# Performance work log

Measured on AMD Instinct MI355X. Metric: run time of the kernel, lower is better.

Reference implementation:

```python
import jax, jax.numpy as jnp
import numpy as np

B, S, D, H = 8, 1024, 1024, 16
HD = D // H  # 64


def setup_inputs() -> dict:
    key = jax.random.key(0)
    ks = jax.random.split(key, 10)
    s = 1.0 / np.sqrt(HD)
    x = jax.random.normal(ks[0], (B, S, D), dtype=jnp.float32)
    mask = jax.random.randint(ks[1], (B, S), 0, 2).astype(bool)  # True = padded
    # per-head q/k/v projections of SimpleAttention, stacked over heads
    Wq = jax.random.normal(ks[2], (H, HD, HD), dtype=jnp.float32) * s
    bq = jnp.zeros((H, HD), dtype=jnp.float32)
    Wk = jax.random.normal(ks[3], (H, HD, HD), dtype=jnp.float32) * s
    bk = jnp.zeros((H, HD), dtype=jnp.float32)
    Wv = jax.random.normal(ks[4], (H, HD, HD), dtype=jnp.float32) * s
    bv = jnp.zeros((H, HD), dtype=jnp.float32)
    # out_proj: Linear(dim, dim)
    Wo = jax.random.normal(ks[5], (D, D), dtype=jnp.float32) * (1.0 / np.sqrt(D))
    bo = jnp.zeros((D,), dtype=jnp.float32)
    return {"x": x, "mask": mask, "Wq": Wq, "bq": bq, "Wk": Wk, "bk": bk,
            "Wv": Wv, "bv": bv, "Wo": Wo, "bo": bo}


def reference(x, mask, Wq, bq, Wk, bk, Wv, bv, Wo, bo):
    b, s, d = x.shape
    xh = x.reshape(b, s, H, HD).transpose(0, 2, 1, 3)  # (b, h, s, hd)
    # per-head linear projections (batched over heads via einsum)
    q = jnp.einsum('bhsd,hde->bhse', xh, Wq) + bq[None, :, None, :]
    k = jnp.einsum('bhsd,hde->bhse', xh, Wk) + bk[None, :, None, :]
    v = jnp.einsum('bhsd,hde->bhse', xh, Wv) + bv[None, :, None, :]
    scale = 1.0 / jnp.sqrt(jnp.asarray(HD, dtype=x.dtype))
    scores = jnp.einsum('bhqd,bhkd->bhqk', q, k) * scale  # (b, h, s, s)
    # key-padding mask: True = padded -> -inf on key axis
    neg = jnp.asarray(jnp.finfo(x.dtype).min, dtype=x.dtype)
    scores = jnp.where(mask[:, None, None, :], neg, scores)
    attn = jax.nn.softmax(scores, axis=-1)
    out = jnp.einsum('bhqk,bhkd->bhqd', attn, v)  # (b, h, s, hd)
    concat = out.transpose(0, 2, 1, 3).reshape(b, s, d)
    # out_proj (dropout is identity in eval)
    return concat @ Wo.T + bo
```

## Files before the change

kernel.cpp:

```cpp
#include <hip/hip_runtime.h>
#include <float.h>

#define B_ 8
#define S_ 1024
#define D_ 1024
#define H_ 16
#define HD_ 64

typedef __attribute__((ext_vector_type(8))) _Float16 half8;
typedef __attribute__((ext_vector_type(4))) _Float16 half4;
typedef __attribute__((ext_vector_type(4))) float f32x4;

__device__ __forceinline__ void gld16(const void* g, void* l) {
  __builtin_amdgcn_global_load_lds(
      (const __attribute__((address_space(1))) void*)g,
      (__attribute__((address_space(3))) void*)l, 16, 0, 0);
}

__global__ __launch_bounds__(256) void prep_kernel(
    const float* __restrict__ Wq, const float* __restrict__ bq,
    const float* __restrict__ Wk, const float* __restrict__ bk,
    const float* __restrict__ Wv, const float* __restrict__ bv,
    const float* __restrict__ Wo, const void* __restrict__ mraw,
    _Float16* __restrict__ Wc, float* __restrict__ bs,
    _Float16* __restrict__ Wo16, float* __restrict__ maskadd) {
  const int bid = blockIdx.x;
  const int tid = threadIdx.x;
  if (bid < 768) {
    const int idx = bid * 256 + tid;
    const int d = idx & 63;
    const int e = (idx >> 6) & 63;
    const int t2 = idx >> 12;
    const int m = t2 % 3, h = t2 / 3;
    const int src = h * 4096 + d * 64 + e;
    float v = (m == 0) ? Wq[src] * 0.18033688f : (m == 1) ? Wk[src] : Wv[src];
    Wc[idx] = (_Float16)v;
    if (idx < 3072) {
      const int mm = idx >> 10, he = idx & 1023;
      float vv = (mm == 0) ? bq[he] * 0.18033688f : (mm == 1) ? bk[he] : bv[he];
      bs[idx] = vv;
    }
  } else if (bid < 800) {
    __shared__ int bad;
    if (tid == 0) bad = 0;
    __syncthreads();
    const unsigned int* mw = (const unsigned int*)mraw;
    int my = 0;
    for (int j = tid; j < 2048; j += 256) my |= (mw[j] & ~1u) ? 1 : 0;
    if (my) atomicOr(&bad, 1);
    __syncthreads();
    const int i = (bid - 768) * 256 + tid;
    const int f = bad;
    const int v = f ? (int)((const unsigned char*)mraw)[i] : ((const int*)mraw)[i];
    maskadd[i] = (v != 0) ? -FLT_MAX : 0.0f;
  } else {
    const int i = (bid - 800) * 256 + tid;
    Wo16[i] = (_Float16)Wo[i];
  }
}

__global__ __launch_bounds__(256) void qkv_kernel(
    const float* __restrict__ x, const _Float16* __restrict__ Wc,
    const float* __restrict__ bs,
    _Float16* __restrict__ q16, _Float16* __restrict__ k16, _Float16* __restrict__ vT16) {
  const int tile = blockIdx.x & 15;
  const int bh = blockIdx.x >> 4;
  const int b = bh >> 4, h = bh & 15;
  const int s0 = tile * 64;
  const int w = threadIdx.x >> 6, lane = threadIdx.x & 63;
  const int col = lane & 15, quad = lane >> 4;
  const int srow = s0 + w * 16 + col;

  const float* xr = x + ((size_t)(b * S_) + srow) * D_ + h * HD_;
  f32x4 x0a = *(const f32x4*)(xr + quad * 8);
  f32x4 x0b = *(const f32x4*)(xr + quad * 8 + 4);
  f32x4 x1a = *(const f32x4*)(xr + 32 + quad * 8);
  f32x4 x1b = *(const f32x4*)(xr + 32 + quad * 8 + 4);
  half8 Xf0, Xf1;
#pragma unroll
  for (int j = 0; j < 4; ++j) {
    Xf0[j] = (_Float16)x0a[j];
    Xf0[4 + j] = (_Float16)x0b[j];
    Xf1[j] = (_Float16)x1a[j];
    Xf1[4 + j] = (_Float16)x1b[j];
  }

  const _Float16* wbase = Wc + (size_t)h * 3 * 4096;
  const f32x4 z4 = {0.f, 0.f, 0.f, 0.f};
#pragma unroll
  for (int mm = 0; mm < 2; ++mm) {
    _Float16* outp = mm ? k16 : q16;
    const _Float16* wm = wbase + mm * 4096;
#pragma unroll
    for (int et = 0; et < 4; ++et) {
      const _Float16* wr = wm + (et * 16 + col) * 64;
      half8 W0 = *(const half8*)(wr + quad * 8);
      half8 W1 = *(const half8*)(wr + 32 + quad * 8);
      f32x4 c = __builtin_amdgcn_mfma_f32_16x16x32_f16(W0, Xf0, z4, 0, 0, 0);
      c = __builtin_amdgcn_mfma_f32_16x16x32_f16(W1, Xf1, c, 0, 0, 0);
      f32x4 bb = *(const f32x4*)(bs + mm * 1024 + h * 64 + et * 16 + quad * 4);
      half4 o;
#pragma unroll
      for (int r = 0; r < 4; ++r) o[r] = (_Float16)(c[r] + bb[r]);
      *(half4*)(outp + ((size_t)bh * S_ + srow) * HD_ + et * 16 + quad * 4) = o;
    }
  }
  {
    const _Float16* wm = wbase + 2 * 4096;
#pragma unroll
    for (int et = 0; et < 4; ++et) {
      const _Float16* wr = wm + (et * 16 + col) * 64;
      half8 W0 = *(const half8*)(wr + quad * 8);
      half8 W1 = *(const half8*)(wr + 32 + quad * 8);
      f32x4 c = __builtin_amdgcn_mfma_f32_16x16x32_f16(Xf0, W0, z4, 0, 0, 0);
      c = __builtin_amdgcn_mfma_f32_16x16x32_f16(Xf1, W1, c, 0, 0, 0);
      float bb = bs[2048 + h * 64 + et * 16 + col];
      half4 o;
#pragma unroll
      for (int r = 0; r < 4; ++r) o[r] = (_Float16)(c[r] + bb);
      *(half4*)(vT16 + ((size_t)bh * HD_ + et * 16 + col) * S_ + s0 + w * 16 + quad * 4) = o;
    }
  }
}

__global__ __launch_bounds__(256, 2) void attn_kernel(
    const _Float16* __restrict__ q, const _Float16* __restrict__ k,
    const _Float16* __restrict__ vT, const float* __restrict__ maskadd,
    _Float16* __restrict__ att) {
  __shared__ alignas(16) _Float16 Ks[2][64 * 64];
  __shared__ alignas(16) _Float16 Vs[2][64 * 64];
  const int bh = blockIdx.x & 127;
  const int qblk = blockIdx.x >> 7;
  const int b = bh >> 4, h = bh & 15;
  const int wv = threadIdx.x >> 6;
  const int lane = threadIdx.x & 63;
  const int quad = lane >> 4, col = lane & 15;
  const int c7 = col & 7;
  const int q0 = qblk * 256 + wv * 64;

  const _Float16* __restrict__ kb = k + (size_t)bh * S_ * HD_;
  const _Float16* __restrict__ vb = vT + (size_t)bh * HD_ * S_;
  const float* __restrict__ mrow = maskadd + b * S_;

  const int jj0 = wv * 128 + lane, jj1 = jj0 + 64;
  const int r0s = jj0 >> 3, r1s = jj1 >> 3;
  const int sg0 = (jj0 & 7) ^ (r0s & 7), sg1 = (jj1 & 7) ^ (r1s & 7);
  const int offK0 = r0s * 128 + sg0 * 16, offK1 = r1s * 128 + sg1 * 16;
  const int offV0 = r0s * 2048 + sg0 * 16, offV1 = r1s * 2048 + sg1 * 16;
  const int ldsb0 = wv * 1024, ldsb1 = wv * 1024 + 512;

  half8 Qf[4][2];
#pragma unroll
  for (int qt = 0; qt < 4; ++qt) {
    const _Float16* qrow = q + ((size_t)bh * S_ + q0 + qt * 16 + col) * HD_;
    Qf[qt][0] = *(const half8*)(qrow + quad * 8);
    Qf[qt][1] = *(const half8*)(qrow + 32 + quad * 8);
  }

  const f32x4 z4 = {0.f, 0.f, 0.f, 0.f};
  f32x4 O[4][4];
#pragma unroll
  for (int qt = 0; qt < 4; ++qt)
#pragma unroll
    for (int et = 0; et < 4; ++et) O[qt][et] = z4;
  float l[4] = {0.f, 0.f, 0.f, 0.f};

  {
    const char* kg = (const char*)kb;
    const char* vg = (const char*)vb;
    gld16(kg + offK0, &Ks[0][ldsb0]);
    gld16(kg + offK1, &Ks[0][ldsb1]);
    gld16(vg + offV0, &Vs[0][ldsb0]);
    gld16(vg + offV1, &Vs[0][ldsb1]);
  }
  int cur = 0;
  for (int c = 0; c < 16; ++c) {
    __syncthreads();
    if (c < 15) {
      const char* kg = (const char*)kb + (size_t)(c + 1) * 8192;
      const char* vg = (const char*)vb + (size_t)(c + 1) * 128;
      gld16(kg + offK0, &Ks[cur ^ 1][ldsb0]);
      gld16(kg + offK1, &Ks[cur ^ 1][ldsb1]);
      gld16(vg + offV0, &Vs[cur ^ 1][ldsb0]);
      gld16(vg + offV1, &Vs[cur ^ 1][ldsb1]);
    }
    const int kk0 = c * 64;
    const _Float16* Kb_ = &Ks[cur][0];
    const _Float16* Vb_ = &Vs[cur][0];
    f32x4 mkv[4];
#pragma unroll
    for (int kt = 0; kt < 4; ++kt) mkv[kt] = *(const f32x4*)(mrow + kk0 + kt * 16 + quad * 4);
    half8 Kf[4][2];
#pragma unroll
    for (int kt = 0; kt < 4; ++kt) {
      const int rb = (kt * 16 + col) * 64;
      Kf[kt][0] = *(const half8*)&Kb_[rb + ((quad) ^ c7) * 8];
      Kf[kt][1] = *(const half8*)&Kb_[rb + ((4 + quad) ^ c7) * 8];
    }
    half4 Vf[4][4];
#pragma unroll
    for (int kt = 0; kt < 4; ++kt) {
      const int sb = ((kt * 2 + (quad >> 1)) ^ c7) * 8 + (quad & 1) * 4;
#pragma unroll
      for (int et = 0; et < 4; ++et) Vf[kt][et] = *(const half4*)&Vb_[(et * 16 + col) * 64 + sb];
    }
#pragma unroll
    for (int qt = 0; qt < 4; ++qt) {
      f32x4 st[4];
#pragma unroll
      for (int kt = 0; kt < 4; ++kt) {
        f32x4 s = __builtin_amdgcn_mfma_f32_16x16x32_f16(Kf[kt][0], Qf[qt][0], mkv[kt], 0, 0, 0);
        st[kt] = __builtin_amdgcn_mfma_f32_16x16x32_f16(Kf[kt][1], Qf[qt][1], s, 0, 0, 0);
      }
      float p[16];
#pragma unroll
      for (int kt = 0; kt < 4; ++kt)
#pragma unroll
        for (int r = 0; r < 4; ++r) p[kt * 4 + r] = __builtin_amdgcn_exp2f(st[kt][r]);
      float s01 = (p[0] + p[1]) + (p[2] + p[3]);
      float s23 = (p[4] + p[5]) + (p[6] + p[7]);
      float s45 = (p[8] + p[9]) + (p[10] + p[11]);
      float s67 = (p[12] + p[13]) + (p[14] + p[15]);
      l[qt] += (s01 + s23) + (s45 + s67);
      half4 ph[4];
#pragma unroll
      for (int kt = 0; kt < 4; ++kt)
#pragma unroll
        for (int r = 0; r < 4; ++r) ph[kt][r] = (_Float16)p[kt * 4 + r];
#pragma unroll
      for (int et = 0; et < 4; ++et) {
        f32x4 o = O[qt][et];
#pragma unroll
        for (int kt = 0; kt < 4; ++kt)
          o = __builtin_amdgcn_mfma_f32_16x16x16f16(Vf[kt][et], ph[kt], o, 0, 0, 0);
        O[qt][et] = o;
      }
    }
    cur ^= 1;
  }
#pragma unroll
  for (int qt = 0; qt < 4; ++qt) {
    float lt = l[qt];
    lt += __shfl_xor(lt, 16);
    lt += __shfl_xor(lt, 32);
    const float inv = 1.0f / lt;
    _Float16* orow = att + ((size_t)(b * S_ + q0 + qt * 16 + col)) * D_ + h * HD_;
#pragma unroll
    for (int et = 0; et < 4; ++et) {
      half4 o;
#pragma unroll
      for (int r = 0; r < 4; ++r) o[r] = (_Float16)(O[qt][et][r] * inv);
      *(half4*)(orow + et * 16 + quad * 4) = o;
    }
  }
}

__global__ __launch_bounds__(256, 4) void outproj_kernel(
    const _Float16* __restrict__ A, const _Float16* __restrict__ Bw,
    const float* __restrict__ bo, float* __restrict__ C) {
  __shared__ alignas(16) _Float16 As[128 * 64];
  __shared__ alignas(16) _Float16 Bs[128 * 64];
  const int m0 = (int)(blockIdx.x >> 3) * 128;
  const int n0 = (int)(blockIdx.x & 7) * 128;
  const int t = threadIdx.x;
  const int lane = t & 63, wv = t >> 6;
  const int quad = lane >> 4, col = lane & 15;
  const int mw = (wv >> 1) * 64, nw = (wv & 1) * 64;

  int rowS[4], segS[4];
#pragma unroll
  for (int sweep = 0; sweep < 4; ++sweep) {
    const int s = sweep * 256 + wv * 64 + lane;
    rowS[sweep] = s >> 3;
    segS[sweep] = (s & 7) ^ (rowS[sweep] & 7);
  }

  f32x4 acc[16];
  const f32x4 z4 = {0.f, 0.f, 0.f, 0.f};
#pragma unroll
  for (int i = 0; i < 16; ++i) acc[i] = z4;

  for (int kt = 0; kt < 16; ++kt) {
#pragma unroll
    for (int sweep = 0; sweep < 4; ++sweep) {
      const int ldsbase = (sweep * 256 + wv * 64) * 8;
      gld16(A + (size_t)(m0 + rowS[sweep]) * D_ + kt * 64 + segS[sweep] * 8, &As[ldsbase]);
      gld16(Bw + (size_t)(n0 + rowS[sweep]) * D_ + kt * 64 + segS[sweep] * 8, &Bs[ldsbase]);
    }
    __syncthreads();
#pragma unroll
    for (int ks = 0; ks < 2; ++ks) {
      half8 aF[4], bF[4];
#pragma unroll
      for (int mt = 0; mt < 4; ++mt) {
        const int row = mw + mt * 16 + col;
        aF[mt] = *(const half8*)&As[row * 64 + (((ks * 4 + quad) ^ (row & 7)) * 8)];
      }
#pragma unroll
      for (int nt = 0; nt < 4; ++nt) {
        const int row = nw + nt * 16 + col;
        bF[nt] = *(const half8*)&Bs[row * 64 + (((ks * 4 + quad) ^ (row & 7)) * 8)];
      }
#pragma unroll
      for (int mt = 0; mt < 4; ++mt)
#pragma unroll
        for (int nt = 0; nt < 4; ++nt)
          acc[mt * 4 + nt] =
              __builtin_amdgcn_mfma_f32_16x16x32_f16(aF[mt], bF[nt], acc[mt * 4 + nt], 0, 0, 0);
    }
    __syncthreads();
  }
#pragma unroll
  for (int mt = 0; mt < 4; ++mt)
#pragma unroll
    for (int nt = 0; nt < 4; ++nt) {
      f32x4 a = acc[mt * 4 + nt];
      const int n = n0 + nw + nt * 16 + col;
      const float bb = bo[n];
#pragma unroll
      for (int r = 0; r < 4; ++r) {
        const int mrow = m0 + mw + mt * 16 + quad * 4 + r;
        C[(size_t)mrow * D_ + n] = a[r] + bb;
      }
    }
}

extern "C" void kernel_launch(void* const* d_in, const int* in_sizes, int n_in,
                              void* d_out, int out_size, void* d_ws, size_t ws_size,
                              hipStream_t stream) {
  const float* x  = (const float*)d_in[0];
  const float* Wq = (const float*)d_in[2];
  const float* bq = (const float*)d_in[3];
  const float* Wk = (const float*)d_in[4];
  const float* bk = (const float*)d_in[5];
  const float* Wv = (const float*)d_in[6];
  const float* bv = (const float*)d_in[7];
  const float* Wo = (const float*)d_in[8];
  const float* bo = (const float*)d_in[9];

  float* wsf     = (float*)d_ws;
  float* maskadd = wsf;
  const size_t NE = (size_t)B_ * H_ * S_ * HD_;
  _Float16* hws  = (_Float16*)(wsf + 16384);
  _Float16* q16  = hws;
  _Float16* k16  = q16 + NE;
  _Float16* vT16 = k16 + NE;
  _Float16* att16 = vT16 + NE;
  _Float16* Wo16 = att16 + NE;
  _Float16* Wc   = Wo16 + 1048576;
  float*    bs   = (float*)(Wc + 196608);

  prep_kernel<<<4896, 256, 0, stream>>>(Wq, bq, Wk, bk, Wv, bv, Wo, d_in[1],
                                        Wc, bs, Wo16, maskadd);
  qkv_kernel<<<B_ * H_ * (S_ / 64), 256, 0, stream>>>(x, Wc, bs, q16, k16, vT16);
  attn_kernel<<<B_ * H_ * (S_ / 256), 256, 0, stream>>>(q16, k16, vT16, maskadd, att16);
  outproj_kernel<<<(B_ * S_ / 128) * (D_ / 128), 256, 0, stream>>>(att16, Wo16, bo, (float*)d_out);
}
```

Baseline: 199.2 us.

## Restructure QKV projection to stage full x rows in LDS, remap outproj blocks

```diff
diff --git a/kernel.cpp b/kernel.cpp
--- a/kernel.cpp
+++ b/kernel.cpp
@@ -63,62 +63,68 @@
     const float* __restrict__ x, const _Float16* __restrict__ Wc,
     const float* __restrict__ bs,
     _Float16* __restrict__ q16, _Float16* __restrict__ k16, _Float16* __restrict__ vT16) {
-  const int tile = blockIdx.x & 15;
-  const int bh = blockIdx.x >> 4;
-  const int b = bh >> 4, h = bh & 15;
-  const int s0 = tile * 64;
-  const int w = threadIdx.x >> 6, lane = threadIdx.x & 63;
+  __shared__ alignas(16) _Float16 Xs[16 * 1024];
+  const int b = blockIdx.x >> 6;
+  const int s0 = (blockIdx.x & 63) * 16;
+  const int t = threadIdx.x;
+  const int lane = t & 63, wv = t >> 6;
   const int col = lane & 15, quad = lane >> 4;
-  const int srow = s0 + w * 16 + col;
-
-  const float* xr = x + ((size_t)(b * S_) + srow) * D_ + h * HD_;
-  f32x4 x0a = *(const f32x4*)(xr + quad * 8);
-  f32x4 x0b = *(const f32x4*)(xr + quad * 8 + 4);
-  f32x4 x1a = *(const f32x4*)(xr + 32 + quad * 8);
-  f32x4 x1b = *(const f32x4*)(xr + 32 + quad * 8 + 4);
-  half8 Xf0, Xf1;
-#pragma unroll
-  for (int j = 0; j < 4; ++j) {
-    Xf0[j] = (_Float16)x0a[j];
-    Xf0[4 + j] = (_Float16)x0b[j];
-    Xf1[j] = (_Float16)x1a[j];
-    Xf1[4 + j] = (_Float16)x1b[j];
-  }
-
-  const _Float16* wbase = Wc + (size_t)h * 3 * 4096;
+
+  for (int j = 0; j < 16; ++j) {
+    f32x4 v = *(const f32x4*)(x + ((size_t)(b * S_) + s0 + j) * D_ + t * 4);
+    half4 hv;
+#pragma unroll
+    for (int r = 0; r < 4; ++r) hv[r] = (_Float16)v[r];
+    const int byte = (t * 8) ^ ((j & 7) << 4);
+    *(half4*)((char*)&Xs[j * 1024] + byte) = hv;
+  }
+  __syncthreads();
+
   const f32x4 z4 = {0.f, 0.f, 0.f, 0.f};
-#pragma unroll
-  for (int mm = 0; mm < 2; ++mm) {
-    _Float16* outp = mm ? k16 : q16;
-    const _Float16* wm = wbase + mm * 4096;
-#pragma unroll
-    for (int et = 0; et < 4; ++et) {
-      const _Float16* wr = wm + (et * 16 + col) * 64;
-      half8 W0 = *(const half8*)(wr + quad * 8);
-      half8 W1 = *(const half8*)(wr + 32 + quad * 8);
-      f32x4 c = __builtin_amdgcn_mfma_f32_16x16x32_f16(W0, Xf0, z4, 0, 0, 0);
-      c = __builtin_amdgcn_mfma_f32_16x16x32_f16(W1, Xf1, c, 0, 0, 0);
-      f32x4 bb = *(const f32x4*)(bs + mm * 1024 + h * 64 + et * 16 + quad * 4);
-      half4 o;
-#pragma unroll
-      for (int r = 0; r < 4; ++r) o[r] = (_Float16)(c[r] + bb[r]);
-      *(half4*)(outp + ((size_t)bh * S_ + srow) * HD_ + et * 16 + quad * 4) = o;
-    }
-  }
-  {
-    const _Float16* wm = wbase + 2 * 4096;
-#pragma unroll
-    for (int et = 0; et < 4; ++et) {
-      const _Float16* wr = wm + (et * 16 + col) * 64;
-      half8 W0 = *(const half8*)(wr + quad * 8);
-      half8 W1 = *(const half8*)(wr + 32 + quad * 8);
-      f32x4 c = __builtin_amdgcn_mfma_f32_16x16x32_f16(Xf0, W0, z4, 0, 0, 0);
-      c = __builtin_amdgcn_mfma_f32_16x16x32_f16(Xf1, W1, c, 0, 0, 0);
-      float bb = bs[2048 + h * 64 + et * 16 + col];
-      half4 o;
-#pragma unroll
-      for (int r = 0; r < 4; ++r) o[r] = (_Float16)(c[r] + bb);
-      *(half4*)(vT16 + ((size_t)bh * HD_ + et * 16 + col) * S_ + s0 + w * 16 + quad * 4) = o;
+  const char* rp = (const char*)&Xs[col * 1024];
+  const int xsw = (col & 7) << 4;
+
+#pragma unroll
+  for (int hi = 0; hi < 4; ++hi) {
+    const int h = wv * 4 + hi;
+    const int bh = (b << 4) | h;
+    const _Float16* wbase = Wc + (size_t)h * 3 * 4096;
+    half8 Xf0 = *(const half8*)(rp + ((h * 128 + quad * 16) ^ xsw));
+    half8 Xf1 = *(const half8*)(rp + ((h * 128 + 64 + quad * 16) ^ xsw));
+#pragma unroll
+    for (int mm = 0; mm < 2; ++mm) {
+      _Float16* outp = mm ? k16 : q16;
+      const _Float16* wm = wbase + mm * 4096;
+#pragma unroll
+      for (int et = 0; et < 4; ++et) {
+        const _Float16* wr = wm + (et * 16 + col) * 64;
+        half8 W0 = *(const half8*)(wr + quad * 8);
+        half8 W1 = *(const half8*)(wr + 32 + quad * 8);
+        f32x4 bb = *(const f32x4*)(bs + mm * 1024 + h * 64 + et * 16 + quad * 4);
+        f32x4 c = __builtin_amdgcn_mfma_f32_16x16x32_f16(W0, Xf0, bb, 0, 0, 0);
+        c = __builtin_amdgcn_mfma_f32_16x16x32_f16(W1, Xf1, c, 0, 0, 0);
+        half4 o;
+#pragma unroll
+        for (int r = 0; r < 4; ++r) o[r] = (_Float16)c[r];
+        *(half4*)(outp + ((size_t)bh * S_ + s0 + col) * HD_ + et * 16 + quad * 4) = o;
+      }
+    }
+    {
+      const _Float16* wm = wbase + 2 * 4096;
+#pragma unroll
+      for (int et = 0; et < 4; ++et) {
+        const _Float16* wr = wm + (et * 16 + col) * 64;
+        half8 W0 = *(const half8*)(wr + quad * 8);
+        half8 W1 = *(const half8*)(wr + 32 + quad * 8);
+        const float bv_ = bs[2048 + h * 64 + et * 16 + col];
+        const f32x4 bb = {bv_, bv_, bv_, bv_};
+        f32x4 c = __builtin_amdgcn_mfma_f32_16x16x32_f16(Xf0, W0, bb, 0, 0, 0);
+        c = __builtin_amdgcn_mfma_f32_16x16x32_f16(Xf1, W1, c, 0, 0, 0);
+        half4 o;
+#pragma unroll
+        for (int r = 0; r < 4; ++r) o[r] = (_Float16)c[r];
+        *(half4*)(vT16 + ((size_t)bh * HD_ + et * 16 + col) * S_ + s0 + quad * 4) = o;
+      }
     }
   }
 }
@@ -260,8 +266,12 @@
     const float* __restrict__ bo, float* __restrict__ C) {
   __shared__ alignas(16) _Float16 As[128 * 64];
   __shared__ alignas(16) _Float16 Bs[128 * 64];
-  const int m0 = (int)(blockIdx.x >> 3) * 128;
-  const int n0 = (int)(blockIdx.x & 7) * 128;
+  const int x_ = blockIdx.x & 7;
+  const int t_ = blockIdx.x >> 3;
+  const int n_ = t_ & 7;
+  const int mlo = t_ >> 3;
+  const int m0 = (x_ * 8 + mlo) * 128;
+  const int n0 = n_ * 128;
   const int t = threadIdx.x;
   const int lane = t & 63, wv = t >> 6;
   const int quad = lane >> 4, col = lane & 15;
@@ -352,7 +362,7 @@
 
   prep_kernel<<<4896, 256, 0, stream>>>(Wq, bq, Wk, bk, Wv, bv, Wo, d_in[1],
                                         Wc, bs, Wo16, maskadd);
-  qkv_kernel<<<B_ * H_ * (S_ / 64), 256, 0, stream>>>(x, Wc, bs, q16, k16, vT16);
+  qkv_kernel<<<B_ * (S_ / 16), 256, 0, stream>>>(x, Wc, bs, q16, k16, vT16);
   attn_kernel<<<B_ * H_ * (S_ / 256), 256, 0, stream>>>(q16, k16, vT16, maskadd, att16);
   outproj_kernel<<<(B_ * S_ / 128) * (D_ / 128), 256, 0, stream>>>(att16, Wo16, bo, (float*)d_out);
 }
```

After: 201.4 us. No clear change (+1.1%).
